# Kernel optimization log

Hardware: AMD Instinct MI355X
Metric: run time of the kernel (lower is better)

## Reference

```python
import jax, jax.numpy as jnp
import numpy as np

# Normalized sobel kernels (kornia normalize_kernel2d: divide by abs-sum = 8)
_SOBEL = np.array([
    [[-1., 0., 1.], [-2., 0., 2.], [-1., 0., 1.]],   # d/dx
    [[-1., -2., -1.], [0., 0., 0.], [1., 2., 1.]],   # d/dy
], dtype=np.float32) / 8.0
_EPS = 1e-6


def _rgb_to_grayscale(x):
    # kornia weights; x: [B,3,H,W] -> [B,1,H,W]
    return 0.299 * x[:, 0:1] + 0.587 * x[:, 1:2] + 0.114 * x[:, 2:3]


def _sobel_edges(x):
    gray = _rgb_to_grayscale(x)
    # replicate padding of 1 (kornia spatial_gradient uses replicate)
    p = jnp.pad(gray, ((0, 0), (0, 0), (1, 1), (1, 1)), mode='edge')
    k = jnp.asarray(_SOBEL)[:, None]  # [2,1,3,3] OIHW
    g = jax.lax.conv_general_dilated(
        p, k, window_strides=(1, 1), padding='VALID',
        dimension_numbers=('NCHW', 'OIHW', 'NCHW'))  # [B,2,H,W]
    # gradient magnitude: sqrt(gx^2 + gy^2 + eps)
    return jnp.sqrt(jnp.sum(g * g, axis=1, keepdims=True) + _EPS)  # [B,1,H,W]


def setup_inputs() -> dict:
    key = jax.random.key(0)
    k1, k2 = jax.random.split(key)
    shape = (16, 3, 512, 512)
    prediction = jax.random.uniform(k1, shape, dtype=jnp.float32)
    target = jax.random.uniform(k2, shape, dtype=jnp.float32)
    return {"prediction": prediction, "target": target}


def reference(prediction, target):
    # forward runs under torch.no_grad() in the original module
    pe = jax.lax.stop_gradient(_sobel_edges(prediction))
    te = jax.lax.stop_gradient(_sobel_edges(target))
    return jnp.mean(jnp.abs(pe - te))  # l1_loss, mean reduction
```

## Files before the change

### kernel.cpp

```cpp
#include <hip/hip_runtime.h>


constexpr int B = 16;
constexpr int H = 512;
constexpr int W = 512;
constexpr int PLANE = H * W;
constexpr int SR = 8;
constexpr int NTHREADS = 256;
constexpr int WAVES_PER_BLOCK = NTHREADS / 64;
constexpr int STRIPS = B * 2 * (H / SR);
constexpr int NBLOCKS = STRIPS / WAVES_PER_BLOCK;
constexpr float EPS = 1e-6f;

__device__ __forceinline__ float4 ldg4(const float* p) {
    return *reinterpret_cast<const float4*>(p);
}

__device__ __forceinline__ float4 gray4(float4 r, float4 g, float4 b) {
    float4 o;
    o.x = 0.299f * r.x + 0.587f * g.x + 0.114f * b.x;
    o.y = 0.299f * r.y + 0.587f * g.y + 0.114f * b.y;
    o.z = 0.299f * r.z + 0.587f * g.z + 0.114f * b.z;
    o.w = 0.299f * r.w + 0.587f * g.w + 0.114f * b.w;
    return o;
}

struct DS { float4 D, S; };

__device__ __forceinline__ DS load_row(
    const float* __restrict__ x0, const float* __restrict__ x1,
    const float* __restrict__ x2,
    int row, int col, int ecol, int lane)
{
    const int off = row * W + col;
    const float4 r = ldg4(x0 + off);
    const float4 g = ldg4(x1 + off);
    const float4 b = ldg4(x2 + off);

    float e = 0.0f;
    if ((lane == 0) | (lane == 63)) {
        const int eo = row * W + ecol;
        e = 0.299f * x0[eo] + 0.587f * x1[eo] + 0.114f * x2[eo];
    }

    const float4 G = gray4(r, g, b);
    float left  = __shfl_up(G.w, 1);
    float right = __shfl_down(G.x, 1);
    if (lane == 0)  left  = e;
    if (lane == 63) right = e;

    DS o;
    o.D.x = G.y - left;
    o.D.y = G.z - G.x;
    o.D.z = G.w - G.y;
    o.D.w = right - G.z;
    o.S.x = left + 2.0f * G.x + G.y;
    o.S.y = G.x  + 2.0f * G.y + G.z;
    o.S.z = G.y  + 2.0f * G.z + G.w;
    o.S.w = G.z  + 2.0f * G.w + right;
    return o;
}

__device__ __forceinline__ float px_loss(
    float dm, float d0, float dp, float sm, float sp,
    float em, float e0, float ep, float qm, float qp)
{
    const float gx = (dm + 2.0f * d0 + dp) * 0.125f;
    const float gy = (sp - sm) * 0.125f;
    const float pe = sqrtf(gx * gx + gy * gy + EPS);
    const float hx = (em + 2.0f * e0 + ep) * 0.125f;
    const float hy = (qp - qm) * 0.125f;
    const float te = sqrtf(hx * hx + hy * hy + EPS);
    return fabsf(pe - te);
}

__global__ __launch_bounds__(NTHREADS, 2) void edge_loss_kernel(
    const float* __restrict__ pred,
    const float* __restrict__ targ,
    float* __restrict__ partial)
{
    const int tid  = threadIdx.x;
    const int lane = tid & 63;
    const int s    = blockIdx.x * WAVES_PER_BLOCK + (tid >> 6);
    const int img  = s >> 7;
    const int half = (s >> 6) & 1;
    const int vs   = s & 63;
    const int r0   = vs * SR;
    const int c0   = half * 256;
    const int col  = c0 + 4 * lane;
    const int ecol = (lane == 0) ? max(c0 - 1, 0) : min(c0 + 256, W - 1);

    const float* __restrict__ p0 = pred + (size_t)img * 3 * PLANE;
    const float* __restrict__ p1 = p0 + PLANE;
    const float* __restrict__ p2 = p0 + 2 * PLANE;
    const float* __restrict__ t0 = targ + (size_t)img * 3 * PLANE;
    const float* __restrict__ t1 = t0 + PLANE;
    const float* __restrict__ t2 = t0 + 2 * PLANE;

    const int rm = max(r0 - 1, 0);
    DS pm = load_row(p0, p1, p2, rm, col, ecol, lane);
    DS tm = load_row(t0, t1, t2, rm, col, ecol, lane);
    DS pc = load_row(p0, p1, p2, r0, col, ecol, lane);
    DS tc = load_row(t0, t1, t2, r0, col, ecol, lane);

    float acc = 0.0f;
    #pragma unroll
    for (int r = 0; r < SR; ++r) {
        const int rp = min(r0 + r + 1, H - 1);
        DS pp = load_row(p0, p1, p2, rp, col, ecol, lane);
        DS tp = load_row(t0, t1, t2, rp, col, ecol, lane);

        acc += px_loss(pm.D.x, pc.D.x, pp.D.x, pm.S.x, pp.S.x,
                       tm.D.x, tc.D.x, tp.D.x, tm.S.x, tp.S.x);
        acc += px_loss(pm.D.y, pc.D.y, pp.D.y, pm.S.y, pp.S.y,
                       tm.D.y, tc.D.y, tp.D.y, tm.S.y, tp.S.y);
        acc += px_loss(pm.D.z, pc.D.z, pp.D.z, pm.S.z, pp.S.z,
                       tm.D.z, tc.D.z, tp.D.z, tm.S.z, tp.S.z);
        acc += px_loss(pm.D.w, pc.D.w, pp.D.w, pm.S.w, pp.S.w,
                       tm.D.w, tc.D.w, tp.D.w, tm.S.w, tp.S.w);

        pm = pc; pc = pp;
        tm = tc; tc = tp;
    }

    #pragma unroll
    for (int off = 32; off > 0; off >>= 1)
        acc += __shfl_down(acc, off);

    if (lane == 0) partial[s] = acc;
}

__global__ __launch_bounds__(256) void reduce_kernel(
    const float* __restrict__ partial,
    float* __restrict__ out)
{
    const int tid = threadIdx.x;
    float acc = 0.0f;
    #pragma unroll
    for (int i = 0; i < STRIPS / 256; ++i)
        acc += partial[tid + i * 256];

    #pragma unroll
    for (int off = 32; off > 0; off >>= 1)
        acc += __shfl_down(acc, off);

    __shared__ float wsum[4];
    if ((tid & 63) == 0) wsum[tid >> 6] = acc;
    __syncthreads();

    if (tid == 0) {
        const float s = wsum[0] + wsum[1] + wsum[2] + wsum[3];
        out[0] = s * (1.0f / (float)((size_t)B * H * W));
    }
}

extern "C" void kernel_launch(void* const* d_in, const int* in_sizes, int n_in,
                              void* d_out, int out_size, void* d_ws, size_t ws_size,
                              hipStream_t stream) {
    const float* pred = (const float*)d_in[0];
    const float* targ = (const float*)d_in[1];
    float* out = (float*)d_out;
    float* partial = (float*)d_ws;

    edge_loss_kernel<<<NBLOCKS, NTHREADS, 0, stream>>>(pred, targ, partial);
    reduce_kernel<<<1, 256, 0, stream>>>(partial, out);
}
```

Before: 131.3 us.

## Give each lane eight columns with halo loads instead of shuffles

Each wave now covers a full 512-wide row strip, with every lane handling 8 columns loaded as two float4s. Neighbour gray values come from scalar halo loads per lane instead of cross-lane shuffles. Blocks shrink to a single 64-thread wave, so there are half as many waves and each does twice the work per row. This removes shuffle traffic and boundary branches, but adds redundant scalar loads, uses more registers per thread, and lowers the number of waves available to hide latency on a memory-bound kernel.

```diff
diff --git a/kernel.cpp b/kernel.cpp
--- a/kernel.cpp
+++ b/kernel.cpp
@@ -6,89 +6,67 @@
 constexpr int W = 512;
 constexpr int PLANE = H * W;
 constexpr int SR = 8;
-constexpr int NTHREADS = 256;
-constexpr int WAVES_PER_BLOCK = NTHREADS / 64;
-constexpr int STRIPS = B * 2 * (H / SR);
-constexpr int NBLOCKS = STRIPS / WAVES_PER_BLOCK;
+constexpr int STRIPS_PER_IMG = H / SR;
+constexpr int NBLOCKS = B * STRIPS_PER_IMG;
 constexpr float EPS = 1e-6f;
 
 __device__ __forceinline__ float4 ldg4(const float* p) {
     return *reinterpret_cast<const float4*>(p);
 }
+__device__ __forceinline__ float grayf(float r, float g, float b) {
+    return 0.299f * r + 0.587f * g + 0.114f * b;
+}
 
-__device__ __forceinline__ float4 gray4(float4 r, float4 g, float4 b) {
-    float4 o;
-    o.x = 0.299f * r.x + 0.587f * g.x + 0.114f * b.x;
-    o.y = 0.299f * r.y + 0.587f * g.y + 0.114f * b.y;
-    o.z = 0.299f * r.z + 0.587f * g.z + 0.114f * b.z;
-    o.w = 0.299f * r.w + 0.587f * g.w + 0.114f * b.w;
+struct RowDS { float D[8]; float S[8]; };
+
+__device__ __forceinline__ RowDS load_row(
+    const float* __restrict__ x0, const float* __restrict__ x1,
+    const float* __restrict__ x2, int rowOff, int cM, int cL, int cR)
+{
+    const int offM = rowOff + cM;
+    const int offL = rowOff + cL;
+    const int offR = rowOff + cR;
+
+    const float4 r0 = ldg4(x0 + offM), r1 = ldg4(x0 + offM + 4);
+    const float4 g0 = ldg4(x1 + offM), g1 = ldg4(x1 + offM + 4);
+    const float4 b0 = ldg4(x2 + offM), b1 = ldg4(x2 + offM + 4);
+    const float lr = x0[offL], lg = x1[offL], lb = x2[offL];
+    const float rr = x0[offR], rg = x1[offR], rb = x2[offR];
+
+    float G[10];
+    G[0] = grayf(lr, lg, lb);
+    G[1] = grayf(r0.x, g0.x, b0.x);
+    G[2] = grayf(r0.y, g0.y, b0.y);
+    G[3] = grayf(r0.z, g0.z, b0.z);
+    G[4] = grayf(r0.w, g0.w, b0.w);
+    G[5] = grayf(r1.x, g1.x, b1.x);
+    G[6] = grayf(r1.y, g1.y, b1.y);
+    G[7] = grayf(r1.z, g1.z, b1.z);
+    G[8] = grayf(r1.w, g1.w, b1.w);
+    G[9] = grayf(rr, rg, rb);
+
+    RowDS o;
+    #pragma unroll
+    for (int c = 0; c < 8; ++c) {
+        o.D[c] = G[c + 2] - G[c];
+        o.S[c] = G[c] + 2.0f * G[c + 1] + G[c + 2];
+    }
     return o;
 }
 
-struct DS { float4 D, S; };
-
-__device__ __forceinline__ DS load_row(
-    const float* __restrict__ x0, const float* __restrict__ x1,
-    const float* __restrict__ x2,
-    int row, int col, int ecol, int lane)
-{
-    const int off = row * W + col;
-    const float4 r = ldg4(x0 + off);
-    const float4 g = ldg4(x1 + off);
-    const float4 b = ldg4(x2 + off);
-
-    float e = 0.0f;
-    if ((lane == 0) | (lane == 63)) {
-        const int eo = row * W + ecol;
-        e = 0.299f * x0[eo] + 0.587f * x1[eo] + 0.114f * x2[eo];
-    }
-
-    const float4 G = gray4(r, g, b);
-    float left  = __shfl_up(G.w, 1);
-    float right = __shfl_down(G.x, 1);
-    if (lane == 0)  left  = e;
-    if (lane == 63) right = e;
-
-    DS o;
-    o.D.x = G.y - left;
-    o.D.y = G.z - G.x;
-    o.D.z = G.w - G.y;
-    o.D.w = right - G.z;
-    o.S.x = left + 2.0f * G.x + G.y;
-    o.S.y = G.x  + 2.0f * G.y + G.z;
-    o.S.z = G.y  + 2.0f * G.z + G.w;
-    o.S.w = G.z  + 2.0f * G.w + right;
-    return o;
-}
-
-__device__ __forceinline__ float px_loss(
-    float dm, float d0, float dp, float sm, float sp,
-    float em, float e0, float ep, float qm, float qp)
-{
-    const float gx = (dm + 2.0f * d0 + dp) * 0.125f;
-    const float gy = (sp - sm) * 0.125f;
-    const float pe = sqrtf(gx * gx + gy * gy + EPS);
-    const float hx = (em + 2.0f * e0 + ep) * 0.125f;
-    const float hy = (qp - qm) * 0.125f;
-    const float te = sqrtf(hx * hx + hy * hy + EPS);
-    return fabsf(pe - te);
-}
-
-__global__ __launch_bounds__(NTHREADS, 2) void edge_loss_kernel(
+__global__ __launch_bounds__(64, 2) void edge_loss_kernel(
     const float* __restrict__ pred,
     const float* __restrict__ targ,
     float* __restrict__ partial)
 {
-    const int tid  = threadIdx.x;
-    const int lane = tid & 63;
-    const int s    = blockIdx.x * WAVES_PER_BLOCK + (tid >> 6);
-    const int img  = s >> 7;
-    const int half = (s >> 6) & 1;
-    const int vs   = s & 63;
+    const int lane = threadIdx.x;
+    const int bid  = blockIdx.x;
+    const int img  = bid >> 6;
+    const int vs   = bid & 63;
     const int r0   = vs * SR;
-    const int c0   = half * 256;
-    const int col  = c0 + 4 * lane;
-    const int ecol = (lane == 0) ? max(c0 - 1, 0) : min(c0 + 256, W - 1);
+    const int cM   = 8 * lane;
+    const int cL   = max(cM - 1, 0);
+    const int cR   = min(cM + 8, W - 1);
 
     const float* __restrict__ p0 = pred + (size_t)img * 3 * PLANE;
     const float* __restrict__ p1 = p0 + PLANE;
@@ -97,28 +75,29 @@
     const float* __restrict__ t1 = t0 + PLANE;
     const float* __restrict__ t2 = t0 + 2 * PLANE;
 
-    const int rm = max(r0 - 1, 0);
-    DS pm = load_row(p0, p1, p2, rm, col, ecol, lane);
-    DS tm = load_row(t0, t1, t2, rm, col, ecol, lane);
-    DS pc = load_row(p0, p1, p2, r0, col, ecol, lane);
-    DS tc = load_row(t0, t1, t2, r0, col, ecol, lane);
+    const int rmOff = max(r0 - 1, 0) * W;
+    RowDS pm = load_row(p0, p1, p2, rmOff, cM, cL, cR);
+    RowDS tm = load_row(t0, t1, t2, rmOff, cM, cL, cR);
+    RowDS pc = load_row(p0, p1, p2, r0 * W, cM, cL, cR);
+    RowDS tc = load_row(t0, t1, t2, r0 * W, cM, cL, cR);
 
     float acc = 0.0f;
     #pragma unroll
     for (int r = 0; r < SR; ++r) {
-        const int rp = min(r0 + r + 1, H - 1);
-        DS pp = load_row(p0, p1, p2, rp, col, ecol, lane);
-        DS tp = load_row(t0, t1, t2, rp, col, ecol, lane);
+        const int rpOff = min(r0 + r + 1, H - 1) * W;
+        RowDS pp = load_row(p0, p1, p2, rpOff, cM, cL, cR);
+        RowDS tp = load_row(t0, t1, t2, rpOff, cM, cL, cR);
 
-        acc += px_loss(pm.D.x, pc.D.x, pp.D.x, pm.S.x, pp.S.x,
-                       tm.D.x, tc.D.x, tp.D.x, tm.S.x, tp.S.x);
-        acc += px_loss(pm.D.y, pc.D.y, pp.D.y, pm.S.y, pp.S.y,
-                       tm.D.y, tc.D.y, tp.D.y, tm.S.y, tp.S.y);
-        acc += px_loss(pm.D.z, pc.D.z, pp.D.z, pm.S.z, pp.S.z,
-                       tm.D.z, tc.D.z, tp.D.z, tm.S.z, tp.S.z);
-        acc += px_loss(pm.D.w, pc.D.w, pp.D.w, pm.S.w, pp.S.w,
-                       tm.D.w, tc.D.w, tp.D.w, tm.S.w, tp.S.w);
-
+        #pragma unroll
+        for (int c = 0; c < 8; ++c) {
+            const float gx = (pm.D[c] + 2.0f * pc.D[c] + pp.D[c]) * 0.125f;
+            const float gy = (pp.S[c] - pm.S[c]) * 0.125f;
+            const float pe = sqrtf(gx * gx + gy * gy + EPS);
+            const float hx = (tm.D[c] + 2.0f * tc.D[c] + tp.D[c]) * 0.125f;
+            const float hy = (tp.S[c] - tm.S[c]) * 0.125f;
+            const float te = sqrtf(hx * hx + hy * hy + EPS);
+            acc += fabsf(pe - te);
+        }
         pm = pc; pc = pp;
         tm = tc; tc = tp;
     }
@@ -127,7 +106,7 @@
     for (int off = 32; off > 0; off >>= 1)
         acc += __shfl_down(acc, off);
 
-    if (lane == 0) partial[s] = acc;
+    if (lane == 0) partial[bid] = acc;
 }
 
 __global__ __launch_bounds__(256) void reduce_kernel(
@@ -137,7 +116,7 @@
     const int tid = threadIdx.x;
     float acc = 0.0f;
     #pragma unroll
-    for (int i = 0; i < STRIPS / 256; ++i)
+    for (int i = 0; i < NBLOCKS / 256; ++i)
         acc += partial[tid + i * 256];
 
     #pragma unroll
@@ -162,6 +141,6 @@
     float* out = (float*)d_out;
     float* partial = (float*)d_ws;
 
-    edge_loss_kernel<<<NBLOCKS, NTHREADS, 0, stream>>>(pred, targ, partial);
+    edge_loss_kernel<<<NBLOCKS, 64, 0, stream>>>(pred, targ, partial);
     reduce_kernel<<<1, 256, 0, stream>>>(partial, out);
 }
```

Result: faster. 123.9 us (-5.7%).
